# Performance work log

Hardware: AMD Instinct MI355X
Metric: run time of the kernel (lower is better)

Reference implementation:

```python
import jax, jax.numpy as jnp
import numpy as np

FEATS = [(100, 100), (50, 50), (25, 25), (13, 13)]  # (W, H) per level
BS, NQ, D = 2, 10000, 256
NH, NL, NP, G = 8, 4, 4, 8
HD = D // NH


def grid_sample_bilinear(im, grid):
    """torch.nn.functional.grid_sample(mode='bilinear', padding_mode='zeros', align_corners=False).
    im: [N, C, H, W]; grid: [N, Hg, Wg, 2] in [-1, 1] (x, y). Returns [N, C, Hg, Wg]."""
    N, C, H, W = im.shape
    Hg, Wg = grid.shape[1], grid.shape[2]
    x = (grid[..., 0] + 1.0) * (W * 0.5) - 0.5
    y = (grid[..., 1] + 1.0) * (H * 0.5) - 0.5
    x0 = jnp.floor(x); y0 = jnp.floor(y)
    wx1 = x - x0; wx0 = 1.0 - wx1
    wy1 = y - y0; wy0 = 1.0 - wy1
    imf = im.reshape(N, C, H * W)

    def corner(xi, yi, w):
        inb = (xi >= 0) & (xi < W) & (yi >= 0) & (yi < H)
        xi_c = jnp.clip(xi, 0, W - 1).astype(jnp.int32)
        yi_c = jnp.clip(yi, 0, H - 1).astype(jnp.int32)
        idx = (yi_c * W + xi_c).reshape(N, 1, Hg * Wg)
        vals = jnp.take_along_axis(imf, idx, axis=2).reshape(N, C, Hg, Wg)
        return vals * (w * inb.astype(im.dtype))[:, None]

    out = (corner(x0, y0, wx0 * wy0) + corner(x0 + 1, y0, wx1 * wy0)
           + corner(x0, y0 + 1, wx0 * wy1) + corner(x0 + 1, y0 + 1, wx1 * wy1))
    return out


def setup_inputs() -> dict:
    key = jax.random.key(0)
    ks = jax.random.split(key, 7)
    nv = sum(w * h for (w, h) in FEATS)
    return {
        "query": jax.random.normal(ks[0], (BS, NQ, D), jnp.float32),
        "value": jax.random.normal(ks[1], (BS, nv, NH, HD), jnp.float32),
        "reference_points": jax.random.uniform(ks[2], (BS, NQ, NL, 2), jnp.float32),
        "spatial_shapes": jnp.array(FEATS, jnp.float32),  # rows are (W, H)
        "W_off": jax.random.normal(ks[3], (NH * NL * NP * 2, D), jnp.float32) * 0.02,
        "b_off": jax.random.normal(ks[4], (NH * NL * NP * 2,), jnp.float32) * 0.5,
        "W_attn": jax.random.normal(ks[5], (NH * NL * NP, D), jnp.float32) * 0.02,
        "b_attn": jax.random.normal(ks[6], (NH * NL * NP,), jnp.float32) * 0.02,
    }


def reference(query, value, reference_points, spatial_shapes, W_off, b_off, W_attn, b_attn):
    bs, nq, _ = query.shape
    # sampling offsets: [bs, nq, NH, NL*NP*2] with (level, point, xy) layout
    off = (jnp.einsum('bqd,od->bqo', query, W_off) + b_off).reshape(bs, nq, NH, NL * NP * 2)
    # reference points tiled to the same (level, point, xy) layout
    ref = jnp.broadcast_to(reference_points[:, :, None, :, None, :],
                           (bs, nq, NH, NL, NP, 2)).reshape(bs, nq, NH, NL * NP * 2)
    # offset normalizer: (1/W, 1/H) per level, tiled over points
    inv = 1.0 / spatial_shapes  # [NL, 2]
    norm = jnp.broadcast_to(inv[:, None, :], (NL, NP, 2)).reshape(-1)
    loc = (ref + off * norm) * 2.0 - 1.0  # [bs, nq, NH, NL*NP*2]
    loc = loc.reshape(bs, nq, NH, NL, NP, 2)

    # attention weights: softmax over (NL*NP), then rearranged to [bs*NH, 1, nq/G, NL*G*NP]
    aw = jax.nn.softmax((jnp.einsum('bqd,od->bqo', query, W_attn) + b_attn)
                        .reshape(bs, nq, NH, NL * NP), axis=-1)
    aw = aw.reshape(bs, nq // G, G, NH, NL, NP).transpose(0, 3, 1, 4, 2, 5)
    aw = aw.reshape(bs * NH, 1, nq // G, NL * G * NP)

    # per-level grid_sample
    sizes = [w * h for (w, h) in FEATS]
    starts = np.concatenate([[0], np.cumsum(sizes)]).tolist()
    sampled = []
    for lvl, (Wl, Hl) in enumerate(FEATS):
        val_l = value[:, starts[lvl]:starts[lvl + 1]]  # [bs, Hl*Wl, NH, HD]
        val_l = val_l.transpose(0, 2, 3, 1).reshape(bs * NH, HD, Hl, Wl)
        grid_l = loc[:, :, :, lvl].transpose(0, 2, 1, 3, 4)  # [bs, NH, nq, NP, 2]
        grid_l = grid_l.reshape(bs * NH, nq // G, G * NP, 2)
        sampled.append(grid_sample_bilinear(val_l, grid_l))  # [bs*NH, HD, nq/G, G*NP]
    sv = jnp.concatenate(sampled, axis=-1)  # [bs*NH, HD, nq/G, NL*G*NP]

    out = sv * aw
    # reduce_sum linear (fixed 0/1 weight from init_weights) == sum over levels and points per group slot
    out = out.reshape(bs * NH, HD, nq // G, NL, G, NP).sum(axis=(3, 5))  # [bs*NH, HD, nq/G, G]
    return out.reshape(bs, NH * HD, nq)
```

## Files before the change

kernel.cpp:

```cpp
#include <hip/hip_runtime.h>

#define NQ   10000
#define BSZ  2
#define DIM  256
#define NH   8
#define HD   32
#define NLV  4
#define NPT  4
#define NV   13294
#define MT   (BSZ*NQ)
#define NOUT 384
#define NVAL (BSZ*NV*NH*HD)
#define GEMM_BLOCKS 939
#define PREP_BLOCKS 6647

typedef float    floatx4 __attribute__((ext_vector_type(4)));
typedef int      intx4   __attribute__((ext_vector_type(4)));
typedef __bf16   bf16x8  __attribute__((ext_vector_type(8)));
typedef _Float16 halfx8  __attribute__((ext_vector_type(8)));
typedef _Float16 halfx4  __attribute__((ext_vector_type(4)));
typedef _Float16 halfx2  __attribute__((ext_vector_type(2)));

__device__ __forceinline__ unsigned pk_bf16(float lo, float hi) {
  return __builtin_amdgcn_perm(__float_as_uint(hi) + 0x8000u,
                               __float_as_uint(lo) + 0x8000u, 0x07060302);
}

__device__ __forceinline__ unsigned short f32_to_f16_bits(float f) {
  _Float16 h = (_Float16)f;
  return __builtin_bit_cast(unsigned short, h);
}

__global__ __launch_bounds__(256) void gp_kernel(
    const float* __restrict__ query, const float* __restrict__ W_off,
    const float* __restrict__ W_attn,
    const float* __restrict__ b_off, const float* __restrict__ b_attn,
    const float* __restrict__ value,
    _Float16* __restrict__ rawh, _Float16* __restrict__ vf16) {
  const int bid = blockIdx.x;
  const int tid = threadIdx.x;
  if (bid >= GEMM_BLOCKS) {
    int i = (bid - GEMM_BLOCKS) * 256 + tid;
    if (i * 4 < NVAL) {
      floatx4 v = *(const floatx4*)&value[i * 4];
      halfx4 t = { (_Float16)v.x, (_Float16)v.y, (_Float16)v.z, (_Float16)v.w };
      *(uint2*)&vf16[i * 4] = *(const uint2*)&t;
    }
    return;
  }
  __shared__ unsigned short As[64][40];
  __shared__ unsigned short Bs[128][40];
  const int n0 = (bid % 3) * 128;
  const int m0 = (bid / 3) * 64;
  const int wave = tid >> 6;
  const int lane = tid & 63;
  const int quad = lane >> 4;
  const int l16  = lane & 15;
  floatx4 acc[8] = {};
  const int ar = tid >> 2;
  const int ac = (tid & 3) * 8;
  const int br = tid >> 1;
  const int bc = (tid & 1) * 16;
  const float* __restrict__ Wsrc =
      (n0 < 256) ? (W_off + (size_t)n0 * DIM) : (W_attn + (size_t)(n0 - 256) * DIM);

  for (int k0 = 0; k0 < DIM; k0 += 32) {
    {
      int gm = m0 + ar;
      floatx4 a0 = {}, a1 = {};
      if (gm < MT) {
        const float* src = query + (size_t)gm * DIM + k0 + ac;
        a0 = *(const floatx4*)src;
        a1 = *(const floatx4*)(src + 4);
      }
      uint4 ua = { pk_bf16(a0.x, a0.y), pk_bf16(a0.z, a0.w),
                   pk_bf16(a1.x, a1.y), pk_bf16(a1.z, a1.w) };
      *(uint4*)&As[ar][ac] = ua;
    }
    {
      const float* src = Wsrc + (size_t)br * DIM + k0 + bc;
      floatx4 b0 = *(const floatx4*)src;
      floatx4 b1 = *(const floatx4*)(src + 4);
      floatx4 b2 = *(const floatx4*)(src + 8);
      floatx4 b3 = *(const floatx4*)(src + 12);
      uint4 u0 = { pk_bf16(b0.x, b0.y), pk_bf16(b0.z, b0.w),
                   pk_bf16(b1.x, b1.y), pk_bf16(b1.z, b1.w) };
      uint4 u1 = { pk_bf16(b2.x, b2.y), pk_bf16(b2.z, b2.w),
                   pk_bf16(b3.x, b3.y), pk_bf16(b3.z, b3.w) };
      *(uint4*)&Bs[br][bc]     = u0;
      *(uint4*)&Bs[br][bc + 8] = u1;
    }
    __syncthreads();
    bf16x8 a = *(const bf16x8*)&As[wave*16 + l16][quad*8];
    #pragma unroll
    for (int nt = 0; nt < 8; nt++) {
      bf16x8 b = *(const bf16x8*)&Bs[nt*16 + l16][quad*8];
      acc[nt] = __builtin_amdgcn_mfma_f32_16x16x32_bf16(a, b, acc[nt], 0, 0, 0);
    }
    __syncthreads();
  }
  #pragma unroll
  for (int nt = 0; nt < 8; nt++) {
    int gn = n0 + nt*16 + l16;
    float bias = (gn < 256) ? b_off[gn] : b_attn[gn - 256];
    #pragma unroll
    for (int r = 0; r < 4; r++) {
      int gm = m0 + wave*16 + quad*4 + r;
      if (gm < MT) rawh[(size_t)gm*NOUT + gn] = (_Float16)(acc[nt][r] + bias);
    }
  }
}

__global__ __launch_bounds__(64, 8) void sample_kernel(
    const _Float16* __restrict__ rawh, const _Float16* __restrict__ vf16,
    const float* __restrict__ refp, _Float16* __restrict__ tmph) {
  const int b  = blockIdx.y;
  const int q0 = blockIdx.x * 2;
  const int mbase = b * NQ + q0;
  const int tid = threadIdx.x;

  __shared__ uint4 s_pk[16 * 17];

  constexpr int WLI[4] = {100, 50, 25, 13};
  constexpr int STI[4] = {0, 10000, 12500, 13125};

  const int p   = tid & 3;
  const int r   = tid >> 2;
  const int hh  = r & 7;
  const int ql0 = r >> 3;
  const int m   = mbase + ql0;
  const _Float16* rp = rawh + (size_t)m * NOUT;

  float lg[4], rpx[4], rpy[4];
  #pragma unroll
  for (int it = 0; it < 4; ++it) {
    unsigned oxy = *(const unsigned*)(rp + hh*32 + it*8 + p*2);
    halfx2 o2 = __builtin_bit_cast(halfx2, oxy);
    lg[it] = (float)rp[256 + hh*16 + it*4 + p];
    float Wl = (float)WLI[it];
    float rx = refp[((size_t)m*NLV + it)*2 + 0];
    float ry = refp[((size_t)m*NLV + it)*2 + 1];
    rpx[it] = rx * Wl + (float)o2.x - 0.5f;
    rpy[it] = ry * Wl + (float)o2.y - 0.5f;
  }

  float mx = fmaxf(fmaxf(lg[0], lg[1]), fmaxf(lg[2], lg[3]));
  mx = fmaxf(mx, __shfl_xor(mx, 1));
  mx = fmaxf(mx, __shfl_xor(mx, 2));
  float e[4], sden = 0.f;
  #pragma unroll
  for (int it = 0; it < 4; ++it) { e[it] = __expf(lg[it] - mx); sden += e[it]; }
  sden += __shfl_xor(sden, 1);
  sden += __shfl_xor(sden, 2);
  float inv = 1.f / sden;

  #pragma unroll
  for (int it = 0; it < 4; ++it) {
    float aw = e[it] * inv;
    float px = rpx[it], py = rpy[it];
    float x0f = floorf(px), y0f = floorf(py);
    int x0 = (int)x0f, y0 = (int)y0f;
    float wx1 = px - x0f, wx0 = 1.f - wx1;
    float wy1 = py - y0f, wy0 = 1.f - wy1;
    const int Wl = WLI[it], STl = STI[it];
    unsigned short ib[4], wb[4];
    #pragma unroll
    for (int t = 0; t < 4; ++t) {
      int xi = x0 + (t & 1), yi = y0 + (t >> 1);
      bool inb = (xi >= 0) & (xi < Wl) & (yi >= 0) & (yi < Wl);
      ib[t] = inb ? (unsigned short)(STl + yi*Wl + xi) : (unsigned short)0;
      float w = inb ? (aw * ((t & 1) ? wx1 : wx0) * ((t >> 1) ? wy1 : wy0)) : 0.f;
      wb[t] = f32_to_f16_bits(w);
    }
    uint4 pk = { (unsigned)ib[0] | ((unsigned)ib[1] << 16),
                 (unsigned)ib[2] | ((unsigned)ib[3] << 16),
                 (unsigned)wb[0] | ((unsigned)wb[1] << 16),
                 (unsigned)wb[2] | ((unsigned)wb[3] << 16) };
    s_pk[r*17 + it*4 + p] = pk;
  }
  __syncthreads();

  const int lane = tid;
  const int ql = lane >> 5;
  const int h = (lane >> 2) & 7, cq = lane & 3;
  const char* vbh = (const char*)vf16 + (size_t)b * (NV*NH*HD*2) + h*64 + cq*16;
  floatx4 acc0 = {0.f,0.f,0.f,0.f}, acc1 = {0.f,0.f,0.f,0.f};
  const int rowbase = (ql*8 + h) * 17;
  #pragma unroll 4
  for (int pt = 0; pt < 16; ++pt) {
    uint4 pk = s_pk[rowbase + pt];
    uint2 wpair = { pk.z, pk.w };
    halfx4 hw = __builtin_bit_cast(halfx4, wpair);
    int o0 = (int)(pk.x & 0xffffu) << 9;
    int o1 = (int)(pk.x >> 16)     << 9;
    int o2 = (int)(pk.y & 0xffffu) << 9;
    int o3 = (int)(pk.y >> 16)     << 9;
    halfx8 v0 = *(const halfx8*)(vbh + o0);
    halfx8 v1 = *(const halfx8*)(vbh + o1);
    halfx8 v2 = *(const halfx8*)(vbh + o2);
    halfx8 v3 = *(const halfx8*)(vbh + o3);
    #pragma unroll
    for (int t = 0; t < 4; ++t) {
      halfx8 v = (t==0) ? v0 : (t==1) ? v1 : (t==2) ? v2 : v3;
      _Float16 wt = hw[t];
      acc0.x += (float)wt * (float)v[0];
      acc0.y += (float)wt * (float)v[1];
      acc0.z += (float)wt * (float)v[2];
      acc0.w += (float)wt * (float)v[3];
      acc1.x += (float)wt * (float)v[4];
      acc1.y += (float)wt * (float)v[5];
      acc1.z += (float)wt * (float)v[6];
      acc1.w += (float)wt * (float)v[7];
    }
  }
  int mo = mbase + ql;
  uint4 st = { __builtin_bit_cast(unsigned, __builtin_amdgcn_cvt_pkrtz(acc0.x, acc0.y)),
               __builtin_bit_cast(unsigned, __builtin_amdgcn_cvt_pkrtz(acc0.z, acc0.w)),
               __builtin_bit_cast(unsigned, __builtin_amdgcn_cvt_pkrtz(acc1.x, acc1.y)),
               __builtin_bit_cast(unsigned, __builtin_amdgcn_cvt_pkrtz(acc1.z, acc1.w)) };
  *(uint4*)&tmph[(size_t)mo * DIM + h*HD + cq*8] = st;
}

__global__ __launch_bounds__(256) void transpose_kernel(
    const _Float16* __restrict__ tmph, float* __restrict__ out) {
  __shared__ float tile[32][33];
  const int b  = blockIdx.z;
  const int q0 = blockIdx.x * 32;
  const int c0 = blockIdx.y * 32;
  const int tx = threadIdx.x & 31;
  const int ty = threadIdx.x >> 5;
  #pragma unroll
  for (int i = 0; i < 4; i++) {
    int qq = q0 + ty + i*8;
    tile[ty + i*8][tx] = (qq < NQ) ? (float)tmph[((size_t)b*NQ + qq)*DIM + c0 + tx] : 0.f;
  }
  __syncthreads();
  if (q0 + tx < NQ) {
    #pragma unroll
    for (int i = 0; i < 4; i++) {
      out[((size_t)b*DIM + c0 + ty + i*8)*NQ + q0 + tx] = tile[tx][ty + i*8];
    }
  }
}

extern "C" void kernel_launch(void* const* d_in, const int* in_sizes, int n_in,
                              void* d_out, int out_size, void* d_ws, size_t ws_size,
                              hipStream_t stream) {
  const float* query  = (const float*)d_in[0];
  const float* value  = (const float*)d_in[1];
  const float* refp   = (const float*)d_in[2];
  const float* W_off  = (const float*)d_in[4];
  const float* b_off  = (const float*)d_in[5];
  const float* W_attn = (const float*)d_in[6];
  const float* b_attn = (const float*)d_in[7];
  float* out = (float*)d_out;

  char* ws = (char*)d_ws;
  _Float16* rawh = (_Float16*)ws;
  _Float16* tmph = (_Float16*)(ws + 15360000);
  _Float16* vf16 = (_Float16*)(ws + 25600000);

  hipLaunchKernelGGL(gp_kernel, dim3(GEMM_BLOCKS + PREP_BLOCKS), dim3(256), 0, stream,
                     query, W_off, W_attn, b_off, b_attn, value, rawh, vf16);
  hipLaunchKernelGGL(sample_kernel, dim3(NQ / 2, BSZ), dim3(64), 0, stream,
                     rawh, vf16, refp, tmph);
  hipLaunchKernelGGL(transpose_kernel, dim3(313, 8, 2), dim3(256), 0, stream,
                     tmph, out);
}
```

Baseline: 176.7 us.

## Fuse output transpose into sample kernel with 16-query blocks

Result: faster. 170.5 us (-3.5%).

```diff
diff --git a/kernel.cpp b/kernel.cpp
--- a/kernel.cpp
+++ b/kernel.cpp
@@ -13,6 +13,7 @@
 #define NVAL (BSZ*NV*NH*HD)
 #define GEMM_BLOCKS 939
 #define PREP_BLOCKS 6647
+#define QPB  16
 
 typedef float    floatx4 __attribute__((ext_vector_type(4)));
 typedef int      intx4   __attribute__((ext_vector_type(4)));
@@ -111,135 +112,145 @@
   }
 }
 
-__global__ __launch_bounds__(64, 8) void sample_kernel(
+union SampleSmem {
+  uint4 pk[16 * 128];
+  float tr[16 * 260];
+};
+
+__global__ __launch_bounds__(256, 5) void sample_kernel(
     const _Float16* __restrict__ rawh, const _Float16* __restrict__ vf16,
-    const float* __restrict__ refp, _Float16* __restrict__ tmph) {
+    const float* __restrict__ refp, float* __restrict__ out) {
   const int b  = blockIdx.y;
-  const int q0 = blockIdx.x * 2;
+  const int q0 = blockIdx.x * QPB;
   const int mbase = b * NQ + q0;
   const int tid = threadIdx.x;
 
-  __shared__ uint4 s_pk[16 * 17];
+  __shared__ SampleSmem sm;
 
   constexpr int WLI[4] = {100, 50, 25, 13};
   constexpr int STI[4] = {0, 10000, 12500, 13125};
 
-  const int p   = tid & 3;
-  const int r   = tid >> 2;
-  const int hh  = r & 7;
-  const int ql0 = r >> 3;
-  const int m   = mbase + ql0;
-  const _Float16* rp = rawh + (size_t)m * NOUT;
-
-  float lg[4], rpx[4], rpy[4];
-  #pragma unroll
-  for (int it = 0; it < 4; ++it) {
-    unsigned oxy = *(const unsigned*)(rp + hh*32 + it*8 + p*2);
-    halfx2 o2 = __builtin_bit_cast(halfx2, oxy);
-    lg[it] = (float)rp[256 + hh*16 + it*4 + p];
-    float Wl = (float)WLI[it];
-    float rx = refp[((size_t)m*NLV + it)*2 + 0];
-    float ry = refp[((size_t)m*NLV + it)*2 + 1];
-    rpx[it] = rx * Wl + (float)o2.x - 0.5f;
-    rpy[it] = ry * Wl + (float)o2.y - 0.5f;
-  }
-
-  float mx = fmaxf(fmaxf(lg[0], lg[1]), fmaxf(lg[2], lg[3]));
-  mx = fmaxf(mx, __shfl_xor(mx, 1));
-  mx = fmaxf(mx, __shfl_xor(mx, 2));
-  float e[4], sden = 0.f;
-  #pragma unroll
-  for (int it = 0; it < 4; ++it) { e[it] = __expf(lg[it] - mx); sden += e[it]; }
-  sden += __shfl_xor(sden, 1);
-  sden += __shfl_xor(sden, 2);
-  float inv = 1.f / sden;
-
-  #pragma unroll
-  for (int it = 0; it < 4; ++it) {
-    float aw = e[it] * inv;
-    float px = rpx[it], py = rpy[it];
-    float x0f = floorf(px), y0f = floorf(py);
-    int x0 = (int)x0f, y0 = (int)y0f;
-    float wx1 = px - x0f, wx0 = 1.f - wx1;
-    float wy1 = py - y0f, wy0 = 1.f - wy1;
-    const int Wl = WLI[it], STl = STI[it];
-    unsigned short ib[4], wb[4];
-    #pragma unroll
-    for (int t = 0; t < 4; ++t) {
-      int xi = x0 + (t & 1), yi = y0 + (t >> 1);
-      bool inb = (xi >= 0) & (xi < Wl) & (yi >= 0) & (yi < Wl);
-      ib[t] = inb ? (unsigned short)(STl + yi*Wl + xi) : (unsigned short)0;
-      float w = inb ? (aw * ((t & 1) ? wx1 : wx0) * ((t >> 1) ? wy1 : wy0)) : 0.f;
-      wb[t] = f32_to_f16_bits(w);
-    }
-    uint4 pk = { (unsigned)ib[0] | ((unsigned)ib[1] << 16),
-                 (unsigned)ib[2] | ((unsigned)ib[3] << 16),
-                 (unsigned)wb[0] | ((unsigned)wb[1] << 16),
-                 (unsigned)wb[2] | ((unsigned)wb[3] << 16) };
-    s_pk[r*17 + it*4 + p] = pk;
+  const int p  = tid & 3;
+  const int r4 = tid >> 2;
+
+  #pragma unroll
+  for (int half = 0; half < 2; ++half) {
+    const int row = half * 64 + r4;
+    const int hh  = row & 7;
+    const int ql0 = row >> 3;
+    const int m   = mbase + ql0;
+    const _Float16* rp = rawh + (size_t)m * NOUT;
+
+    float lg[4], rpx[4], rpy[4];
+    #pragma unroll
+    for (int it = 0; it < 4; ++it) {
+      unsigned oxy = *(const unsigned*)(rp + hh*32 + it*8 + p*2);
+      halfx2 o2 = __builtin_bit_cast(halfx2, oxy);
+      lg[it] = (float)rp[256 + hh*16 + it*4 + p];
+      float Wl = (float)WLI[it];
+      float rx = refp[((size_t)m*NLV + it)*2 + 0];
+      float ry = refp[((size_t)m*NLV + it)*2 + 1];
+      rpx[it] = rx * Wl + (float)o2.x - 0.5f;
+      rpy[it] = ry * Wl + (float)o2.y - 0.5f;
+    }
+
+    float mx = fmaxf(fmaxf(lg[0], lg[1]), fmaxf(lg[2], lg[3]));
+    mx = fmaxf(mx, __shfl_xor(mx, 1));
+    mx = fmaxf(mx, __shfl_xor(mx, 2));
+    float e[4], sden = 0.f;
+    #pragma unroll
+    for (int it = 0; it < 4; ++it) { e[it] = __expf(lg[it] - mx); sden += e[it]; }
+    sden += __shfl_xor(sden, 1);
+    sden += __shfl_xor(sden, 2);
+    float inv = 1.f / sden;
+
+    #pragma unroll
+    for (int it = 0; it < 4; ++it) {
+      float aw = e[it] * inv;
+      float px = rpx[it], py = rpy[it];
+      float x0f = floorf(px), y0f = floorf(py);
+      int x0 = (int)x0f, y0 = (int)y0f;
+      float wx1 = px - x0f, wx0 = 1.f - wx1;
+      float wy1 = py - y0f, wy0 = 1.f - wy1;
+      const int Wl = WLI[it], STl = STI[it];
+      unsigned short ib[4], wb[4];
+      #pragma unroll
+      for (int t = 0; t < 4; ++t) {
+        int xi = x0 + (t & 1), yi = y0 + (t >> 1);
+        bool inb = (xi >= 0) & (xi < Wl) & (yi >= 0) & (yi < Wl);
+        ib[t] = inb ? (unsigned short)(STl + yi*Wl + xi) : (unsigned short)0;
+        float w = inb ? (aw * ((t & 1) ? wx1 : wx0) * ((t >> 1) ? wy1 : wy0)) : 0.f;
+        wb[t] = f32_to_f16_bits(w);
+      }
+      uint4 pk = { (unsigned)ib[0] | ((unsigned)ib[1] << 16),
+                   (unsigned)ib[2] | ((unsigned)ib[3] << 16),
+                   (unsigned)wb[0] | ((unsigned)wb[1] << 16),
+                   (unsigned)wb[2] | ((unsigned)wb[3] << 16) };
+      sm.pk[(it*4 + p)*128 + row] = pk;
+    }
   }
   __syncthreads();
 
-  const int lane = tid;
-  const int ql = lane >> 5;
-  const int h = (lane >> 2) & 7, cq = lane & 3;
+  const int wv = tid >> 6, lane = tid & 63;
+  const int qh = lane >> 5;
+  const int h  = (lane >> 2) & 7, cq = lane & 3;
   const char* vbh = (const char*)vf16 + (size_t)b * (NV*NH*HD*2) + h*64 + cq*16;
-  floatx4 acc0 = {0.f,0.f,0.f,0.f}, acc1 = {0.f,0.f,0.f,0.f};
-  const int rowbase = (ql*8 + h) * 17;
-  #pragma unroll 4
-  for (int pt = 0; pt < 16; ++pt) {
-    uint4 pk = s_pk[rowbase + pt];
-    uint2 wpair = { pk.z, pk.w };
-    halfx4 hw = __builtin_bit_cast(halfx4, wpair);
-    int o0 = (int)(pk.x & 0xffffu) << 9;
-    int o1 = (int)(pk.x >> 16)     << 9;
-    int o2 = (int)(pk.y & 0xffffu) << 9;
-    int o3 = (int)(pk.y >> 16)     << 9;
-    halfx8 v0 = *(const halfx8*)(vbh + o0);
-    halfx8 v1 = *(const halfx8*)(vbh + o1);
-    halfx8 v2 = *(const halfx8*)(vbh + o2);
-    halfx8 v3 = *(const halfx8*)(vbh + o3);
-    #pragma unroll
-    for (int t = 0; t < 4; ++t) {
-      halfx8 v = (t==0) ? v0 : (t==1) ? v1 : (t==2) ? v2 : v3;
-      _Float16 wt = hw[t];
-      acc0.x += (float)wt * (float)v[0];
-      acc0.y += (float)wt * (float)v[1];
-      acc0.z += (float)wt * (float)v[2];
-      acc0.w += (float)wt * (float)v[3];
-      acc1.x += (float)wt * (float)v[4];
-      acc1.y += (float)wt * (float)v[5];
-      acc1.z += (float)wt * (float)v[6];
-      acc1.w += (float)wt * (float)v[7];
-    }
-  }
-  int mo = mbase + ql;
-  uint4 st = { __builtin_bit_cast(unsigned, __builtin_amdgcn_cvt_pkrtz(acc0.x, acc0.y)),
-               __builtin_bit_cast(unsigned, __builtin_amdgcn_cvt_pkrtz(acc0.z, acc0.w)),
-               __builtin_bit_cast(unsigned, __builtin_amdgcn_cvt_pkrtz(acc1.x, acc1.y)),
-               __builtin_bit_cast(unsigned, __builtin_amdgcn_cvt_pkrtz(acc1.z, acc1.w)) };
-  *(uint4*)&tmph[(size_t)mo * DIM + h*HD + cq*8] = st;
-}
-
-__global__ __launch_bounds__(256) void transpose_kernel(
-    const _Float16* __restrict__ tmph, float* __restrict__ out) {
-  __shared__ float tile[32][33];
-  const int b  = blockIdx.z;
-  const int q0 = blockIdx.x * 32;
-  const int c0 = blockIdx.y * 32;
-  const int tx = threadIdx.x & 31;
-  const int ty = threadIdx.x >> 5;
-  #pragma unroll
-  for (int i = 0; i < 4; i++) {
-    int qq = q0 + ty + i*8;
-    tile[ty + i*8][tx] = (qq < NQ) ? (float)tmph[((size_t)b*NQ + qq)*DIM + c0 + tx] : 0.f;
+  floatx4 accs[2][2];
+  #pragma unroll
+  for (int pass = 0; pass < 2; ++pass) {
+    const int ql   = wv*4 + pass*2 + qh;
+    const int rowb = ql*8 + h;
+    floatx4 a0 = {0.f,0.f,0.f,0.f}, a1 = {0.f,0.f,0.f,0.f};
+    #pragma unroll 4
+    for (int pt = 0; pt < 16; ++pt) {
+      uint4 pk = sm.pk[pt*128 + rowb];
+      uint2 wpair = { pk.z, pk.w };
+      halfx4 hw = __builtin_bit_cast(halfx4, wpair);
+      int o0 = (int)(pk.x & 0xffffu) << 9;
+      int o1 = (int)(pk.x >> 16)     << 9;
+      int o2 = (int)(pk.y & 0xffffu) << 9;
+      int o3 = (int)(pk.y >> 16)     << 9;
+      halfx8 v0 = *(const halfx8*)(vbh + o0);
+      halfx8 v1 = *(const halfx8*)(vbh + o1);
+      halfx8 v2 = *(const halfx8*)(vbh + o2);
+      halfx8 v3 = *(const halfx8*)(vbh + o3);
+      #pragma unroll
+      for (int t = 0; t < 4; ++t) {
+        halfx8 v = (t==0) ? v0 : (t==1) ? v1 : (t==2) ? v2 : v3;
+        _Float16 wt = hw[t];
+        a0.x += (float)wt * (float)v[0];
+        a0.y += (float)wt * (float)v[1];
+        a0.z += (float)wt * (float)v[2];
+        a0.w += (float)wt * (float)v[3];
+        a1.x += (float)wt * (float)v[4];
+        a1.y += (float)wt * (float)v[5];
+        a1.z += (float)wt * (float)v[6];
+        a1.w += (float)wt * (float)v[7];
+      }
+    }
+    accs[pass][0] = a0;
+    accs[pass][1] = a1;
   }
   __syncthreads();
-  if (q0 + tx < NQ) {
-    #pragma unroll
-    for (int i = 0; i < 4; i++) {
-      out[((size_t)b*DIM + c0 + ty + i*8)*NQ + q0 + tx] = tile[tx][ty + i*8];
-    }
+
+  #pragma unroll
+  for (int pass = 0; pass < 2; ++pass) {
+    const int ql  = wv*4 + pass*2 + qh;
+    const int ch0 = h*32 + cq*8;
+    *(floatx4*)&sm.tr[ql*260 + ch0]     = accs[pass][0];
+    *(floatx4*)&sm.tr[ql*260 + ch0 + 4] = accs[pass][1];
+  }
+  __syncthreads();
+  {
+    const int ch = tid;
+    float vals[QPB];
+    #pragma unroll
+    for (int q = 0; q < QPB; ++q) vals[q] = sm.tr[q*260 + ch];
+    float* op = out + ((size_t)b*DIM + ch)*NQ + q0;
+    *(floatx4*)&op[0]  = *(const floatx4*)&vals[0];
+    *(floatx4*)&op[4]  = *(const floatx4*)&vals[4];
+    *(floatx4*)&op[8]  = *(const floatx4*)&vals[8];
+    *(floatx4*)&op[12] = *(const floatx4*)&vals[12];
   }
 }
 
@@ -257,13 +268,10 @@
 
   char* ws = (char*)d_ws;
   _Float16* rawh = (_Float16*)ws;
-  _Float16* tmph = (_Float16*)(ws + 15360000);
-  _Float16* vf16 = (_Float16*)(ws + 25600000);
+  _Float16* vf16 = (_Float16*)(ws + 15360000);
 
   hipLaunchKernelGGL(gp_kernel, dim3(GEMM_BLOCKS + PREP_BLOCKS), dim3(256), 0, stream,
                      query, W_off, W_attn, b_off, b_attn, value, rawh, vf16);
-  hipLaunchKernelGGL(sample_kernel, dim3(NQ / 2, BSZ), dim3(64), 0, stream,
-                     rawh, vf16, refp, tmph);
-  hipLaunchKernelGGL(transpose_kernel, dim3(313, 8, 2), dim3(256), 0, stream,
-                     tmph, out);
-}
+  hipLaunchKernelGGL(sample_kernel, dim3(NQ / QPB, BSZ), dim3(256), 0, stream,
+                     rawh, vf16, refp, out);
+}
```
